# Optimization experiments

Measured on AMD Instinct MI355X. Metric: run time of the kernel, lower is better.

## Reference

```python
import jax, jax.numpy as jnp
import numpy as np

N, M = 8192, 128  # n samples, m features


def setup_inputs() -> dict:
    key = jax.random.key(0)
    k0, k1, k2, k3, k4 = jax.random.split(key, 5)
    L = jax.random.normal(k0, (N, M), dtype=jnp.float32)
    X = jax.random.normal(k1, (N, M), dtype=jnp.float32)
    Y = jax.random.normal(k2, (N,), dtype=jnp.float32)
    # params of the sub-network `net` (modeled as Linear(m, m))
    Wnet = jax.random.normal(k3, (M, M), dtype=jnp.float32) / np.float32(np.sqrt(M))
    bnet = jax.random.normal(k4, (M,), dtype=jnp.float32) * 0.01
    return {"L": L, "X": X, "Y": Y, "Wnet": Wnet, "bnet": bnet}


def reference(L, X, Y, Wnet, bnet):
    # A[i] = L[i] * X[i];  B[j] = net(X[j]) * X[j]   (elementwise feature weighting)
    A = L * X                                    # [n, m]
    B = (X @ Wnet + bnet) * X                    # [n, m] -- net(X[j]) computed once, batched
    # pairwise L2 distances: dist[i,j] = ||A_i - B_j||
    d2 = (jnp.sum(A * A, axis=1)[:, None]
          + jnp.sum(B * B, axis=1)[None, :]
          - 2.0 * (A @ B.T))                     # [n, n]
    dist = jnp.sqrt(jnp.maximum(d2, 1e-12))
    drum = jnp.exp(-dist)                        # [n, n] kernel weights
    # Nadaraya-Watson prediction: pred_i = (drum_i . Y) / sum_j drum_ij
    pred = (drum @ Y) / jnp.sum(drum, axis=1)    # [n]
    return jnp.sum((Y - pred) ** 2)              # scalar loss
```

## Files before the change

### kernel.cpp

```cpp
#include <hip/hip_runtime.h>
#include <hip/hip_bf16.h>
#include <cstdint>


#define N_ 8192
#define M_ 128
#define K2_ 2.0813689810056077f
#define NEG2K2_ -4.1627379620112154f

typedef __bf16 bf16x8 __attribute__((ext_vector_type(8)));
typedef float  f32x4  __attribute__((ext_vector_type(4)));

__device__ __forceinline__ unsigned short f2bf(float f) {
    unsigned int x = __float_as_uint(f);
    unsigned int r = x + 0x7fffu + ((x >> 16) & 1u);
    return (unsigned short)(r >> 16);
}

__device__ __forceinline__ void async_cp16(const void* g, void* l) {
    __builtin_amdgcn_global_load_lds(
        (const __attribute__((address_space(1))) void*)g,
        (__attribute__((address_space(3))) void*)l, 16, 0, 0);
}


__global__ __launch_bounds__(256) void prep_kernel(
    const float* __restrict__ L, const float* __restrict__ X,
    const float* __restrict__ Y, const float* __restrict__ Wnet,
    const float* __restrict__ bnet,
    unsigned short* __restrict__ Asw, unsigned short* __restrict__ Bsw,
    float* __restrict__ naS, float2* __restrict__ nbY,
    float* __restrict__ sumw, float* __restrict__ sumwy)
{
    __shared__ float Xs[16][128];
    const int tid  = threadIdx.x;
    const int row0 = blockIdx.x * 16;
    const int k4   = tid & 31;
    const int rr   = tid >> 5;

    #pragma unroll
    for (int i = 0; i < 2; ++i)
        ((float4*)Xs)[tid + i * 256] =
            ((const float4*)(X + (size_t)row0 * 128))[tid + i * 256];
    __syncthreads();

    float acc0[4] = {0.f, 0.f, 0.f, 0.f};
    float acc1[4] = {0.f, 0.f, 0.f, 0.f};
    const int r0 = rr * 2, r1 = rr * 2 + 1;
    #pragma unroll 4
    for (int c = 0; c < 128; ++c) {
        float4 w4 = *(const float4*)(Wnet + c * 128 + k4 * 4);
        float x0 = Xs[r0][c], x1 = Xs[r1][c];
        acc0[0] = fmaf(x0, w4.x, acc0[0]); acc1[0] = fmaf(x1, w4.x, acc1[0]);
        acc0[1] = fmaf(x0, w4.y, acc0[1]); acc1[1] = fmaf(x1, w4.y, acc1[1]);
        acc0[2] = fmaf(x0, w4.z, acc0[2]); acc1[2] = fmaf(x1, w4.z, acc1[2]);
        acc0[3] = fmaf(x0, w4.w, acc0[3]); acc1[3] = fmaf(x1, w4.w, acc1[3]);
    }

    const float4 bn4 = *(const float4*)(bnet + k4 * 4);
    float napart[2], nbpart[2];
    #pragma unroll
    for (int j = 0; j < 2; ++j) {
        const int ln  = rr * 2 + j;
        const int row = row0 + ln;
        const float* acc = j ? acc1 : acc0;
        const float4 xv = *(const float4*)(&Xs[ln][k4 * 4]);
        const float4 l4 = *(const float4*)(L + (size_t)row * 128 + k4 * 4);
        unsigned short apk[4], bpk[4];
        float nA_ = 0.f, nB_ = 0.f;
        const float xe[4] = {xv.x, xv.y, xv.z, xv.w};
        const float le[4] = {l4.x, l4.y, l4.z, l4.w};
        const float be[4] = {bn4.x, bn4.y, bn4.z, bn4.w};
        #pragma unroll
        for (int e = 0; e < 4; ++e) {
            float a = le[e] * xe[e];
            float b = (acc[e] + be[e]) * xe[e];
            unsigned short ua = f2bf(a), ub = f2bf(b);
            apk[e] = ua; bpk[e] = ub;
            float af = __uint_as_float((unsigned)ua << 16);
            float bf = __uint_as_float((unsigned)ub << 16);
            nA_ = fmaf(af, af, nA_);
            nB_ = fmaf(bf, bf, nB_);
        }
        napart[j] = nA_; nbpart[j] = nB_;
        size_t off = (size_t)blockIdx.x * 2048 + (size_t)(k4 >> 3) * 512
                   + (size_t)((k4 >> 1) & 3) * 128 + (size_t)ln * 8 + (k4 & 1) * 4;
        uint2 pa = make_uint2((unsigned)apk[0] | ((unsigned)apk[1] << 16),
                              (unsigned)apk[2] | ((unsigned)apk[3] << 16));
        uint2 pb = make_uint2((unsigned)bpk[0] | ((unsigned)bpk[1] << 16),
                              (unsigned)bpk[2] | ((unsigned)bpk[3] << 16));
        *(uint2*)(Asw + off) = pa;
        *(uint2*)(Bsw + off) = pb;
    }

    #pragma unroll
    for (int m = 1; m <= 16; m <<= 1) {
        napart[0] += __shfl_xor(napart[0], m, 64);
        napart[1] += __shfl_xor(napart[1], m, 64);
        nbpart[0] += __shfl_xor(nbpart[0], m, 64);
        nbpart[1] += __shfl_xor(nbpart[1], m, 64);
    }
    if (k4 == 0) {
        #pragma unroll
        for (int j = 0; j < 2; ++j) {
            int row = row0 + rr * 2 + j;
            naS[row] = K2_ * napart[j];
            nbY[row] = make_float2(K2_ * nbpart[j], Y[row]);
        }
    }
    if (tid < 16) sumw[row0 + tid] = 0.f;
    else if (tid < 32) sumwy[row0 + tid - 16] = 0.f;
}

__global__ __launch_bounds__(256) void pairwise_kernel(
    const unsigned short* __restrict__ Asw, const unsigned short* __restrict__ Bsw,
    const float* __restrict__ naS, const float2* __restrict__ nbY,
    float* __restrict__ sumw, float* __restrict__ sumwy)
{
    __shared__ __align__(16) unsigned short ldsB[16384];
    __shared__ __align__(16) float2 ldsNbY[512];

    const int tid  = threadIdx.x;
    const int wv   = tid >> 6;
    const int lane = tid & 63;
    const int ln16 = lane & 15;
    const int quad = lane >> 4;
    const int i0   = blockIdx.x * 128;
    const int j0   = blockIdx.y * 512;

    ((float4*)ldsNbY)[tid] = ((const float4*)(nbY + j0))[tid];

    bf16x8 afrag[2][4];
    float  na[2][4];
    #pragma unroll
    for (int rt = 0; rt < 2; ++rt) {
        const int gA = (i0 >> 4) + wv * 2 + rt;
        const unsigned short* ap = Asw + (size_t)gA * 2048 + lane * 8;
        #pragma unroll
        for (int ks = 0; ks < 4; ++ks)
            afrag[rt][ks] = *(const bf16x8*)(ap + ks * 512);
        #pragma unroll
        for (int r = 0; r < 4; ++r)
            na[rt][r] = naS[gA * 16 + quad * 4 + r];
    }

    float accw[2][4], accwy[2][4];
    #pragma unroll
    for (int rt = 0; rt < 2; ++rt)
        #pragma unroll
        for (int r = 0; r < 4; ++r) { accw[rt][r] = 0.f; accwy[rt][r] = 0.f; }

    for (int jt = 0; jt < 4; ++jt) {
        {
            const unsigned short* gsrc = Bsw + (size_t)(j0 >> 4) * 2048
                                       + (size_t)jt * 16384 + wv * 4096 + lane * 8;
            unsigned short* ldst = ldsB + wv * 4096;
            #pragma unroll
            for (int i = 0; i < 8; ++i)
                async_cp16(gsrc + i * 512, ldst + i * 512);
        }
        __syncthreads();

        #pragma unroll 2
        for (int ct = 0; ct < 8; ++ct) {
            bf16x8 bfrag[4];
            const unsigned short* bp = ldsB + ct * 2048 + lane * 8;
            #pragma unroll
            for (int ks = 0; ks < 4; ++ks)
                bfrag[ks] = *(const bf16x8*)(bp + ks * 512);
            const float2 nv = ldsNbY[jt * 128 + ct * 16 + ln16];

            #pragma unroll
            for (int rt = 0; rt < 2; ++rt) {
                f32x4 s = {0.f, 0.f, 0.f, 0.f};
                #pragma unroll
                for (int ks = 0; ks < 4; ++ks)
                    s = __builtin_amdgcn_mfma_f32_16x16x32_bf16(
                            afrag[rt][ks], bfrag[ks], s, 0, 0, 0);
                #pragma unroll
                for (int r = 0; r < 4; ++r) {
                    float d2 = fmaf(NEG2K2_, s[r], na[rt][r] + nv.x);
                    d2 = fmaxf(d2, 0.f);
                    float w = __builtin_amdgcn_exp2f(-__builtin_amdgcn_sqrtf(d2));
                    accw[rt][r] += w;
                    accwy[rt][r] = fmaf(w, nv.y, accwy[rt][r]);
                }
            }
        }
        __syncthreads();
    }

    #pragma unroll
    for (int rt = 0; rt < 2; ++rt)
        #pragma unroll
        for (int r = 0; r < 4; ++r) {
            float w  = accw[rt][r];
            float wy = accwy[rt][r];
            #pragma unroll
            for (int m = 1; m <= 8; m <<= 1) {
                w  += __shfl_xor(w,  m, 64);
                wy += __shfl_xor(wy, m, 64);
            }
            if (ln16 == 0) {
                int row = i0 + wv * 32 + rt * 16 + quad * 4 + r;
                atomicAdd(&sumw[row],  w);
                atomicAdd(&sumwy[row], wy);
            }
        }
}

__global__ __launch_bounds__(1024) void finish_kernel(
    const float* __restrict__ Y, const float* __restrict__ sumw,
    const float* __restrict__ sumwy, float* __restrict__ out)
{
    __shared__ float red[16];
    const int tid = threadIdx.x;
    float acc = 0.f;
    #pragma unroll
    for (int i = 0; i < 2; ++i) {
        int idx = tid + i * 1024;
        float4 w4  = ((const float4*)sumw)[idx];
        float4 wy4 = ((const float4*)sumwy)[idx];
        float4 y4  = ((const float4*)Y)[idx];
        const float we[4]  = {w4.x, w4.y, w4.z, w4.w};
        const float wye[4] = {wy4.x, wy4.y, wy4.z, wy4.w};
        const float ye[4]  = {y4.x, y4.y, y4.z, y4.w};
        #pragma unroll
        for (int e = 0; e < 4; ++e) {
            float pred = wye[e] * __builtin_amdgcn_rcpf(we[e]);
            float d = ye[e] - pred;
            acc = fmaf(d, d, acc);
        }
    }
    #pragma unroll
    for (int m = 1; m < 64; m <<= 1) acc += __shfl_xor(acc, m, 64);
    if ((tid & 63) == 0) red[tid >> 6] = acc;
    __syncthreads();
    if (tid < 64) {
        float v = (tid < 16) ? red[tid] : 0.f;
        #pragma unroll
        for (int m = 1; m < 16; m <<= 1) v += __shfl_xor(v, m, 64);
        if (tid == 0) out[0] = v;
    }
}

extern "C" void kernel_launch(void* const* d_in, const int* in_sizes, int n_in,
                              void* d_out, int out_size, void* d_ws, size_t ws_size,
                              hipStream_t stream)
{
    const float* L    = (const float*)d_in[0];
    const float* X    = (const float*)d_in[1];
    const float* Y    = (const float*)d_in[2];
    const float* Wnet = (const float*)d_in[3];
    const float* bnet = (const float*)d_in[4];
    float* out = (float*)d_out;

    char* ws = (char*)d_ws;
    unsigned short* Asw = (unsigned short*)(ws);
    unsigned short* Bsw = (unsigned short*)(ws + (size_t)2 * 1024 * 1024);
    float*  naS   = (float*) (ws + (size_t)4 * 1024 * 1024);
    float2* nbYp  = (float2*)(ws + (size_t)4 * 1024 * 1024 + 32 * 1024);
    float*  sumw  = (float*) (ws + (size_t)4 * 1024 * 1024 + 96 * 1024);
    float*  sumwy = (float*) (ws + (size_t)4 * 1024 * 1024 + 128 * 1024);

    prep_kernel<<<N_ / 16, 256, 0, stream>>>(L, X, Y, Wnet, bnet,
                                             Asw, Bsw, naS, nbYp, sumw, sumwy);
    pairwise_kernel<<<dim3(N_ / 128, 16), 256, 0, stream>>>(Asw, Bsw, naS, nbYp,
                                                            sumw, sumwy);
    finish_kernel<<<1, 1024, 0, stream>>>(Y, sumw, sumwy, out);
}
```

Measured before the change: 105.6 us.

## Load B fragments directly from global memory and stage Wnet in LDS

The pairwise kernel drops its LDS staging of B tiles and nbY, along with the barriers, and instead loads MFMA B fragments and norms directly from global memory (cached) inside one 32-iteration loop. It also sets a launch-bounds occupancy hint of 4 blocks per CU. The prep kernel copies the whole Wnet matrix into 64KB of LDS and reads four columns at a time with vector loads. The goals are to remove barrier stalls and async-copy overhead and to raise occupancy, at the cost of relying on L1/L2 to hold the B fragments that every wave re-reads.

```diff
diff --git a/kernel.cpp b/kernel.cpp
--- a/kernel.cpp
+++ b/kernel.cpp
@@ -15,12 +15,6 @@
     unsigned int x = __float_as_uint(f);
     unsigned int r = x + 0x7fffu + ((x >> 16) & 1u);
     return (unsigned short)(r >> 16);
-}
-
-__device__ __forceinline__ void async_cp16(const void* g, void* l) {
-    __builtin_amdgcn_global_load_lds(
-        (const __attribute__((address_space(1))) void*)g,
-        (__attribute__((address_space(3))) void*)l, 16, 0, 0);
 }
 
 
@@ -32,6 +26,7 @@
     float* __restrict__ naS, float2* __restrict__ nbY,
     float* __restrict__ sumw, float* __restrict__ sumwy)
 {
+    __shared__ float Ws[128 * 128];
     __shared__ float Xs[16][128];
     const int tid  = threadIdx.x;
     const int row0 = blockIdx.x * 16;
@@ -39,6 +34,9 @@
     const int rr   = tid >> 5;
 
     #pragma unroll
+    for (int i = 0; i < 16; ++i)
+        ((float4*)Ws)[tid + i * 256] = ((const float4*)Wnet)[tid + i * 256];
+    #pragma unroll
     for (int i = 0; i < 2; ++i)
         ((float4*)Xs)[tid + i * 256] =
             ((const float4*)(X + (size_t)row0 * 128))[tid + i * 256];
@@ -47,14 +45,28 @@
     float acc0[4] = {0.f, 0.f, 0.f, 0.f};
     float acc1[4] = {0.f, 0.f, 0.f, 0.f};
     const int r0 = rr * 2, r1 = rr * 2 + 1;
-    #pragma unroll 4
-    for (int c = 0; c < 128; ++c) {
-        float4 w4 = *(const float4*)(Wnet + c * 128 + k4 * 4);
-        float x0 = Xs[r0][c], x1 = Xs[r1][c];
-        acc0[0] = fmaf(x0, w4.x, acc0[0]); acc1[0] = fmaf(x1, w4.x, acc1[0]);
-        acc0[1] = fmaf(x0, w4.y, acc0[1]); acc1[1] = fmaf(x1, w4.y, acc1[1]);
-        acc0[2] = fmaf(x0, w4.z, acc0[2]); acc1[2] = fmaf(x1, w4.z, acc1[2]);
-        acc0[3] = fmaf(x0, w4.w, acc0[3]); acc1[3] = fmaf(x1, w4.w, acc1[3]);
+    #pragma unroll 2
+    for (int c4 = 0; c4 < 128; c4 += 4) {
+        const float4 x0 = *(const float4*)&Xs[r0][c4];
+        const float4 x1 = *(const float4*)&Xs[r1][c4];
+        const float4 wc0 = *(const float4*)&Ws[(c4 + 0) * 128 + k4 * 4];
+        const float4 wc1 = *(const float4*)&Ws[(c4 + 1) * 128 + k4 * 4];
+        const float4 wc2 = *(const float4*)&Ws[(c4 + 2) * 128 + k4 * 4];
+        const float4 wc3 = *(const float4*)&Ws[(c4 + 3) * 128 + k4 * 4];
+        const float x0e[4] = {x0.x, x0.y, x0.z, x0.w};
+        const float x1e[4] = {x1.x, x1.y, x1.z, x1.w};
+        const float4 wce[4] = {wc0, wc1, wc2, wc3};
+        #pragma unroll
+        for (int c = 0; c < 4; ++c) {
+            acc0[0] = fmaf(x0e[c], wce[c].x, acc0[0]);
+            acc0[1] = fmaf(x0e[c], wce[c].y, acc0[1]);
+            acc0[2] = fmaf(x0e[c], wce[c].z, acc0[2]);
+            acc0[3] = fmaf(x0e[c], wce[c].w, acc0[3]);
+            acc1[0] = fmaf(x1e[c], wce[c].x, acc1[0]);
+            acc1[1] = fmaf(x1e[c], wce[c].y, acc1[1]);
+            acc1[2] = fmaf(x1e[c], wce[c].z, acc1[2]);
+            acc1[3] = fmaf(x1e[c], wce[c].w, acc1[3]);
+        }
     }
 
     const float4 bn4 = *(const float4*)(bnet + k4 * 4);
@@ -112,14 +124,11 @@
     else if (tid < 32) sumwy[row0 + tid - 16] = 0.f;
 }
 
-__global__ __launch_bounds__(256) void pairwise_kernel(
+__global__ __launch_bounds__(256, 4) void pairwise_kernel(
     const unsigned short* __restrict__ Asw, const unsigned short* __restrict__ Bsw,
     const float* __restrict__ naS, const float2* __restrict__ nbY,
     float* __restrict__ sumw, float* __restrict__ sumwy)
 {
-    __shared__ __align__(16) unsigned short ldsB[16384];
-    __shared__ __align__(16) float2 ldsNbY[512];
-
     const int tid  = threadIdx.x;
     const int wv   = tid >> 6;
     const int lane = tid & 63;
@@ -128,8 +137,6 @@
     const int i0   = blockIdx.x * 128;
     const int j0   = blockIdx.y * 512;
 
-    ((float4*)ldsNbY)[tid] = ((const float4*)(nbY + j0))[tid];
-
     bf16x8 afrag[2][4];
     float  na[2][4];
     #pragma unroll
@@ -150,44 +157,34 @@
         #pragma unroll
         for (int r = 0; r < 4; ++r) { accw[rt][r] = 0.f; accwy[rt][r] = 0.f; }
 
-    for (int jt = 0; jt < 4; ++jt) {
-        {
-            const unsigned short* gsrc = Bsw + (size_t)(j0 >> 4) * 2048
-                                       + (size_t)jt * 16384 + wv * 4096 + lane * 8;
-            unsigned short* ldst = ldsB + wv * 4096;
-            #pragma unroll
-            for (int i = 0; i < 8; ++i)
-                async_cp16(gsrc + i * 512, ldst + i * 512);
-        }
-        __syncthreads();
-
-        #pragma unroll 2
-        for (int ct = 0; ct < 8; ++ct) {
-            bf16x8 bfrag[4];
-            const unsigned short* bp = ldsB + ct * 2048 + lane * 8;
+    const unsigned short* bbase = Bsw + (size_t)(j0 >> 4) * 2048 + lane * 8;
+    const float2* nbbase = nbY + j0 + ln16;
+
+    #pragma unroll 4
+    for (int ct = 0; ct < 32; ++ct) {
+        const unsigned short* bp = bbase + (size_t)ct * 2048;
+        bf16x8 bfrag[4];
+        #pragma unroll
+        for (int ks = 0; ks < 4; ++ks)
+            bfrag[ks] = *(const bf16x8*)(bp + ks * 512);
+        const float2 nv = nbbase[ct * 16];
+
+        #pragma unroll
+        for (int rt = 0; rt < 2; ++rt) {
+            f32x4 s = {0.f, 0.f, 0.f, 0.f};
             #pragma unroll
             for (int ks = 0; ks < 4; ++ks)
-                bfrag[ks] = *(const bf16x8*)(bp + ks * 512);
-            const float2 nv = ldsNbY[jt * 128 + ct * 16 + ln16];
-
+                s = __builtin_amdgcn_mfma_f32_16x16x32_bf16(
+                        afrag[rt][ks], bfrag[ks], s, 0, 0, 0);
             #pragma unroll
-            for (int rt = 0; rt < 2; ++rt) {
-                f32x4 s = {0.f, 0.f, 0.f, 0.f};
-                #pragma unroll
-                for (int ks = 0; ks < 4; ++ks)
-                    s = __builtin_amdgcn_mfma_f32_16x16x32_bf16(
-                            afrag[rt][ks], bfrag[ks], s, 0, 0, 0);
-                #pragma unroll
-                for (int r = 0; r < 4; ++r) {
-                    float d2 = fmaf(NEG2K2_, s[r], na[rt][r] + nv.x);
-                    d2 = fmaxf(d2, 0.f);
-                    float w = __builtin_amdgcn_exp2f(-__builtin_amdgcn_sqrtf(d2));
-                    accw[rt][r] += w;
-                    accwy[rt][r] = fmaf(w, nv.y, accwy[rt][r]);
-                }
+            for (int r = 0; r < 4; ++r) {
+                float d2 = fmaf(NEG2K2_, s[r], na[rt][r] + nv.x);
+                d2 = fmaxf(d2, 0.f);
+                float w = __builtin_amdgcn_exp2f(-__builtin_amdgcn_sqrtf(d2));
+                accw[rt][r] += w;
+                accwy[rt][r] = fmaf(w, nv.y, accwy[rt][r]);
             }
         }
-        __syncthreads();
     }
 
     #pragma unroll
```

After: 105.5 us. Within noise of the previous version (-0.1%).

## Drop LDS staging in pairwise kernel, load B fragments directly with register double-buffering

Applied to the files above, without the earlier changes.

The pairwise kernel no longer stages B tiles into LDS with async copies and barriers. Each wave now reads its B fragments straight from global memory (L2) into two register buffers that are prefetched one step ahead. Each block covers 64 rows instead of 128 with one row tile per wave, and the kernel gets an occupancy hint of 6. The prep kernel moves to 64-thread blocks with a 4x8 register tile and packs bf16 pairs with 16-byte stores. The trade is more L2 traffic per block and a doubled grid, in return for no barriers and higher occupancy.

```diff
diff --git a/kernel.cpp b/kernel.cpp
--- a/kernel.cpp
+++ b/kernel.cpp
@@ -4,27 +4,23 @@
 
 
 #define N_ 8192
-#define M_ 128
 #define K2_ 2.0813689810056077f
 #define NEG2K2_ -4.1627379620112154f
 
 typedef __bf16 bf16x8 __attribute__((ext_vector_type(8)));
 typedef float  f32x4  __attribute__((ext_vector_type(4)));
 
-__device__ __forceinline__ unsigned short f2bf(float f) {
-    unsigned int x = __float_as_uint(f);
-    unsigned int r = x + 0x7fffu + ((x >> 16) & 1u);
-    return (unsigned short)(r >> 16);
-}
-
-__device__ __forceinline__ void async_cp16(const void* g, void* l) {
-    __builtin_amdgcn_global_load_lds(
-        (const __attribute__((address_space(1))) void*)g,
-        (__attribute__((address_space(3))) void*)l, 16, 0, 0);
-}
-
-
-__global__ __launch_bounds__(256) void prep_kernel(
+
+__device__ __forceinline__ uint32_t rne2(float f0, float f1, float& r0, float& r1) {
+    uint32_t u0 = __float_as_uint(f0), u1 = __float_as_uint(f1);
+    uint32_t t0 = u0 + 0x7fffu + ((u0 >> 16) & 1u);
+    uint32_t t1 = u1 + 0x7fffu + ((u1 >> 16) & 1u);
+    r0 = __uint_as_float(t0 & 0xffff0000u);
+    r1 = __uint_as_float(t1 & 0xffff0000u);
+    return (t0 >> 16) | (t1 & 0xffff0000u);
+}
+
+__global__ __launch_bounds__(64) void prep_kernel(
     const float* __restrict__ L, const float* __restrict__ X,
     const float* __restrict__ Y, const float* __restrict__ Wnet,
     const float* __restrict__ bnet,
@@ -35,178 +31,192 @@
     __shared__ float Xs[16][128];
     const int tid  = threadIdx.x;
     const int row0 = blockIdx.x * 16;
-    const int k4   = tid & 31;
-    const int rr   = tid >> 5;
-
-    #pragma unroll
-    for (int i = 0; i < 2; ++i)
-        ((float4*)Xs)[tid + i * 256] =
-            ((const float4*)(X + (size_t)row0 * 128))[tid + i * 256];
+    const int rg   = tid >> 4;
+    const int cg   = tid & 15;
+
+    #pragma unroll
+    for (int i = 0; i < 8; ++i)
+        ((float4*)Xs)[tid + i * 64] =
+            ((const float4*)(X + (size_t)row0 * 128))[tid + i * 64];
+    if (tid < 16) sumw[row0 + tid] = 0.f;
+    else if (tid < 32) sumwy[row0 + tid - 16] = 0.f;
     __syncthreads();
 
-    float acc0[4] = {0.f, 0.f, 0.f, 0.f};
-    float acc1[4] = {0.f, 0.f, 0.f, 0.f};
-    const int r0 = rr * 2, r1 = rr * 2 + 1;
+    float acc[4][8];
+    #pragma unroll
+    for (int r = 0; r < 4; ++r)
+        #pragma unroll
+        for (int e = 0; e < 8; ++e) acc[r][e] = 0.f;
+
     #pragma unroll 4
     for (int c = 0; c < 128; ++c) {
-        float4 w4 = *(const float4*)(Wnet + c * 128 + k4 * 4);
-        float x0 = Xs[r0][c], x1 = Xs[r1][c];
-        acc0[0] = fmaf(x0, w4.x, acc0[0]); acc1[0] = fmaf(x1, w4.x, acc1[0]);
-        acc0[1] = fmaf(x0, w4.y, acc0[1]); acc1[1] = fmaf(x1, w4.y, acc1[1]);
-        acc0[2] = fmaf(x0, w4.z, acc0[2]); acc1[2] = fmaf(x1, w4.z, acc1[2]);
-        acc0[3] = fmaf(x0, w4.w, acc0[3]); acc1[3] = fmaf(x1, w4.w, acc1[3]);
-    }
-
-    const float4 bn4 = *(const float4*)(bnet + k4 * 4);
-    float napart[2], nbpart[2];
-    #pragma unroll
-    for (int j = 0; j < 2; ++j) {
-        const int ln  = rr * 2 + j;
+        const float4 w0 = *(const float4*)(Wnet + c * 128 + cg * 8);
+        const float4 w1 = *(const float4*)(Wnet + c * 128 + cg * 8 + 4);
+        const float we[8] = {w0.x, w0.y, w0.z, w0.w, w1.x, w1.y, w1.z, w1.w};
+        #pragma unroll
+        for (int r = 0; r < 4; ++r) {
+            const float xv = Xs[rg * 4 + r][c];
+            #pragma unroll
+            for (int e = 0; e < 8; ++e)
+                acc[r][e] = fmaf(xv, we[e], acc[r][e]);
+        }
+    }
+
+    const float4 bn0 = *(const float4*)(bnet + cg * 8);
+    const float4 bn1 = *(const float4*)(bnet + cg * 8 + 4);
+    const float bne[8] = {bn0.x, bn0.y, bn0.z, bn0.w, bn1.x, bn1.y, bn1.z, bn1.w};
+    const int ks = cg >> 2, quad = cg & 3;
+
+    float napart[4], nbpart[4];
+    #pragma unroll
+    for (int r = 0; r < 4; ++r) {
+        const int ln  = rg * 4 + r;
         const int row = row0 + ln;
-        const float* acc = j ? acc1 : acc0;
-        const float4 xv = *(const float4*)(&Xs[ln][k4 * 4]);
-        const float4 l4 = *(const float4*)(L + (size_t)row * 128 + k4 * 4);
-        unsigned short apk[4], bpk[4];
-        float nA_ = 0.f, nB_ = 0.f;
-        const float xe[4] = {xv.x, xv.y, xv.z, xv.w};
-        const float le[4] = {l4.x, l4.y, l4.z, l4.w};
-        const float be[4] = {bn4.x, bn4.y, bn4.z, bn4.w};
-        #pragma unroll
-        for (int e = 0; e < 4; ++e) {
-            float a = le[e] * xe[e];
-            float b = (acc[e] + be[e]) * xe[e];
-            unsigned short ua = f2bf(a), ub = f2bf(b);
-            apk[e] = ua; bpk[e] = ub;
-            float af = __uint_as_float((unsigned)ua << 16);
-            float bf = __uint_as_float((unsigned)ub << 16);
-            nA_ = fmaf(af, af, nA_);
-            nB_ = fmaf(bf, bf, nB_);
-        }
-        napart[j] = nA_; nbpart[j] = nB_;
-        size_t off = (size_t)blockIdx.x * 2048 + (size_t)(k4 >> 3) * 512
-                   + (size_t)((k4 >> 1) & 3) * 128 + (size_t)ln * 8 + (k4 & 1) * 4;
-        uint2 pa = make_uint2((unsigned)apk[0] | ((unsigned)apk[1] << 16),
-                              (unsigned)apk[2] | ((unsigned)apk[3] << 16));
-        uint2 pb = make_uint2((unsigned)bpk[0] | ((unsigned)bpk[1] << 16),
-                              (unsigned)bpk[2] | ((unsigned)bpk[3] << 16));
-        *(uint2*)(Asw + off) = pa;
-        *(uint2*)(Bsw + off) = pb;
-    }
-
-    #pragma unroll
-    for (int m = 1; m <= 16; m <<= 1) {
-        napart[0] += __shfl_xor(napart[0], m, 64);
-        napart[1] += __shfl_xor(napart[1], m, 64);
-        nbpart[0] += __shfl_xor(nbpart[0], m, 64);
-        nbpart[1] += __shfl_xor(nbpart[1], m, 64);
-    }
-    if (k4 == 0) {
-        #pragma unroll
-        for (int j = 0; j < 2; ++j) {
-            int row = row0 + rr * 2 + j;
-            naS[row] = K2_ * napart[j];
-            nbY[row] = make_float2(K2_ * nbpart[j], Y[row]);
-        }
-    }
-    if (tid < 16) sumw[row0 + tid] = 0.f;
-    else if (tid < 32) sumwy[row0 + tid - 16] = 0.f;
-}
-
-__global__ __launch_bounds__(256) void pairwise_kernel(
+        const float4 x0 = *(const float4*)(&Xs[ln][cg * 8]);
+        const float4 x1 = *(const float4*)(&Xs[ln][cg * 8 + 4]);
+        const float4 l0 = *(const float4*)(L + (size_t)row * 128 + cg * 8);
+        const float4 l1 = *(const float4*)(L + (size_t)row * 128 + cg * 8 + 4);
+        const float xe[8] = {x0.x, x0.y, x0.z, x0.w, x1.x, x1.y, x1.z, x1.w};
+        const float le[8] = {l0.x, l0.y, l0.z, l0.w, l1.x, l1.y, l1.z, l1.w};
+        uint32_t pa[4], pb[4];
+        float na_ = 0.f, nb_ = 0.f;
+        #pragma unroll
+        for (int h = 0; h < 4; ++h) {
+            float a0 = le[2 * h] * xe[2 * h];
+            float a1 = le[2 * h + 1] * xe[2 * h + 1];
+            float b0 = (acc[r][2 * h] + bne[2 * h]) * xe[2 * h];
+            float b1 = (acc[r][2 * h + 1] + bne[2 * h + 1]) * xe[2 * h + 1];
+            float ra0, ra1, rb0, rb1;
+            pa[h] = rne2(a0, a1, ra0, ra1);
+            pb[h] = rne2(b0, b1, rb0, rb1);
+            na_ = fmaf(ra0, ra0, na_); na_ = fmaf(ra1, ra1, na_);
+            nb_ = fmaf(rb0, rb0, nb_); nb_ = fmaf(rb1, rb1, nb_);
+        }
+        napart[r] = na_; nbpart[r] = nb_;
+        size_t off = (size_t)blockIdx.x * 2048 + (size_t)ks * 512
+                   + (size_t)quad * 128 + (size_t)ln * 8;
+        *(uint4*)(Asw + off) = make_uint4(pa[0], pa[1], pa[2], pa[3]);
+        *(uint4*)(Bsw + off) = make_uint4(pb[0], pb[1], pb[2], pb[3]);
+    }
+
+    #pragma unroll
+    for (int m = 1; m <= 8; m <<= 1) {
+        #pragma unroll
+        for (int r = 0; r < 4; ++r) {
+            napart[r] += __shfl_xor(napart[r], m, 64);
+            nbpart[r] += __shfl_xor(nbpart[r], m, 64);
+        }
+    }
+    if (cg == 0) {
+        #pragma unroll
+        for (int r = 0; r < 4; ++r) {
+            int row = row0 + rg * 4 + r;
+            naS[row] = K2_ * napart[r];
+            nbY[row] = make_float2(K2_ * nbpart[r], Y[row]);
+        }
+    }
+}
+
+__global__ __launch_bounds__(256, 6) void pairwise_kernel(
     const unsigned short* __restrict__ Asw, const unsigned short* __restrict__ Bsw,
     const float* __restrict__ naS, const float2* __restrict__ nbY,
     float* __restrict__ sumw, float* __restrict__ sumwy)
 {
-    __shared__ __align__(16) unsigned short ldsB[16384];
-    __shared__ __align__(16) float2 ldsNbY[512];
-
     const int tid  = threadIdx.x;
     const int wv   = tid >> 6;
     const int lane = tid & 63;
     const int ln16 = lane & 15;
     const int quad = lane >> 4;
-    const int i0   = blockIdx.x * 128;
+    const int i0   = blockIdx.x * 64;
     const int j0   = blockIdx.y * 512;
-
-    ((float4*)ldsNbY)[tid] = ((const float4*)(nbY + j0))[tid];
-
-    bf16x8 afrag[2][4];
-    float  na[2][4];
-    #pragma unroll
-    for (int rt = 0; rt < 2; ++rt) {
-        const int gA = (i0 >> 4) + wv * 2 + rt;
+    const int gA   = (i0 >> 4) + wv;
+
+    bf16x8 afrag[4];
+    {
         const unsigned short* ap = Asw + (size_t)gA * 2048 + lane * 8;
         #pragma unroll
-        for (int ks = 0; ks < 4; ++ks)
-            afrag[rt][ks] = *(const bf16x8*)(ap + ks * 512);
-        #pragma unroll
-        for (int r = 0; r < 4; ++r)
-            na[rt][r] = naS[gA * 16 + quad * 4 + r];
-    }
-
-    float accw[2][4], accwy[2][4];
-    #pragma unroll
-    for (int rt = 0; rt < 2; ++rt)
-        #pragma unroll
-        for (int r = 0; r < 4; ++r) { accw[rt][r] = 0.f; accwy[rt][r] = 0.f; }
-
-    for (int jt = 0; jt < 4; ++jt) {
+        for (int ksi = 0; ksi < 4; ++ksi)
+            afrag[ksi] = *(const bf16x8*)(ap + ksi * 512);
+    }
+    float na[4];
+    #pragma unroll
+    for (int r = 0; r < 4; ++r)
+        na[r] = naS[gA * 16 + quad * 4 + r];
+
+    float accw[4] = {0.f, 0.f, 0.f, 0.f};
+    float accwy[4] = {0.f, 0.f, 0.f, 0.f};
+
+    const unsigned short* bbase = Bsw + (size_t)(j0 >> 4) * 2048 + lane * 8;
+    const float2* nbb = nbY + j0 + ln16;
+
+    bf16x8 b0[4], b1[4];
+    float2 nv0, nv1;
+    #pragma unroll
+    for (int ksi = 0; ksi < 4; ++ksi) {
+        b0[ksi] = *(const bf16x8*)(bbase + ksi * 512);
+        b1[ksi] = *(const bf16x8*)(bbase + 2048 + ksi * 512);
+    }
+    nv0 = nbb[0];
+    nv1 = nbb[16];
+
+    for (int ct = 0; ct < 32; ct += 2) {
         {
-            const unsigned short* gsrc = Bsw + (size_t)(j0 >> 4) * 2048
-                                       + (size_t)jt * 16384 + wv * 4096 + lane * 8;
-            unsigned short* ldst = ldsB + wv * 4096;
-            #pragma unroll
-            for (int i = 0; i < 8; ++i)
-                async_cp16(gsrc + i * 512, ldst + i * 512);
-        }
-        __syncthreads();
-
-        #pragma unroll 2
-        for (int ct = 0; ct < 8; ++ct) {
-            bf16x8 bfrag[4];
-            const unsigned short* bp = ldsB + ct * 2048 + lane * 8;
-            #pragma unroll
-            for (int ks = 0; ks < 4; ++ks)
-                bfrag[ks] = *(const bf16x8*)(bp + ks * 512);
-            const float2 nv = ldsNbY[jt * 128 + ct * 16 + ln16];
-
-            #pragma unroll
-            for (int rt = 0; rt < 2; ++rt) {
-                f32x4 s = {0.f, 0.f, 0.f, 0.f};
-                #pragma unroll
-                for (int ks = 0; ks < 4; ++ks)
-                    s = __builtin_amdgcn_mfma_f32_16x16x32_bf16(
-                            afrag[rt][ks], bfrag[ks], s, 0, 0, 0);
-                #pragma unroll
-                for (int r = 0; r < 4; ++r) {
-                    float d2 = fmaf(NEG2K2_, s[r], na[rt][r] + nv.x);
-                    d2 = fmaxf(d2, 0.f);
-                    float w = __builtin_amdgcn_exp2f(-__builtin_amdgcn_sqrtf(d2));
-                    accw[rt][r] += w;
-                    accwy[rt][r] = fmaf(w, nv.y, accwy[rt][r]);
-                }
+            f32x4 s = {0.f, 0.f, 0.f, 0.f};
+            #pragma unroll
+            for (int ksi = 0; ksi < 4; ++ksi)
+                s = __builtin_amdgcn_mfma_f32_16x16x32_bf16(afrag[ksi], b0[ksi], s, 0, 0, 0);
+            const unsigned short* bp = bbase + (size_t)(ct + 2) * 2048;
+            const float yj = nv0.y, nb = nv0.x;
+            #pragma unroll
+            for (int ksi = 0; ksi < 4; ++ksi)
+                b0[ksi] = *(const bf16x8*)(bp + ksi * 512);
+            nv0 = nbb[(ct + 2) * 16];
+            #pragma unroll
+            for (int r = 0; r < 4; ++r) {
+                float d2 = fmaf(NEG2K2_, s[r], na[r] + nb);
+                d2 = fmaxf(d2, 0.f);
+                float w = __builtin_amdgcn_exp2f(-__builtin_amdgcn_sqrtf(d2));
+                accw[r] += w;
+                accwy[r] = fmaf(w, yj, accwy[r]);
             }
         }
-        __syncthreads();
-    }
-
-    #pragma unroll
-    for (int rt = 0; rt < 2; ++rt)
-        #pragma unroll
-        for (int r = 0; r < 4; ++r) {
-            float w  = accw[rt][r];
-            float wy = accwy[rt][r];
-            #pragma unroll
-            for (int m = 1; m <= 8; m <<= 1) {
-                w  += __shfl_xor(w,  m, 64);
-                wy += __shfl_xor(wy, m, 64);
+        {
+            f32x4 s = {0.f, 0.f, 0.f, 0.f};
+            #pragma unroll
+            for (int ksi = 0; ksi < 4; ++ksi)
+                s = __builtin_amdgcn_mfma_f32_16x16x32_bf16(afrag[ksi], b1[ksi], s, 0, 0, 0);
+            const unsigned short* bp = bbase + (size_t)(ct + 3) * 2048;
+            const float yj = nv1.y, nb = nv1.x;
+            #pragma unroll
+            for (int ksi = 0; ksi < 4; ++ksi)
+                b1[ksi] = *(const bf16x8*)(bp + ksi * 512);
+            nv1 = nbb[(ct + 3) * 16];
+            #pragma unroll
+            for (int r = 0; r < 4; ++r) {
+                float d2 = fmaf(NEG2K2_, s[r], na[r] + nb);
+                d2 = fmaxf(d2, 0.f);
+                float w = __builtin_amdgcn_exp2f(-__builtin_amdgcn_sqrtf(d2));
+                accw[r] += w;
+                accwy[r] = fmaf(w, yj, accwy[r]);
             }
-            if (ln16 == 0) {
-                int row = i0 + wv * 32 + rt * 16 + quad * 4 + r;
-                atomicAdd(&sumw[row],  w);
-                atomicAdd(&sumwy[row], wy);
-            }
-        }
+        }
+    }
+
+    #pragma unroll
+    for (int r = 0; r < 4; ++r) {
+        float w  = accw[r];
+        float wy = accwy[r];
+        #pragma unroll
+        for (int m = 1; m <= 8; m <<= 1) {
+            w  += __shfl_xor(w,  m, 64);
+            wy += __shfl_xor(wy, m, 64);
+        }
+        if (ln16 == 0) {
+            int row = i0 + wv * 16 + quad * 4 + r;
+            atomicAdd(&sumw[row],  w);
+            atomicAdd(&sumwy[row], wy);
+        }
+    }
 }
 
 __global__ __launch_bounds__(1024) void finish_kernel(
@@ -263,9 +273,9 @@
     float*  sumw  = (float*) (ws + (size_t)4 * 1024 * 1024 + 96 * 1024);
     float*  sumwy = (float*) (ws + (size_t)4 * 1024 * 1024 + 128 * 1024);
 
-    prep_kernel<<<N_ / 16, 256, 0, stream>>>(L, X, Y, Wnet, bnet,
-                                             Asw, Bsw, naS, nbYp, sumw, sumwy);
-    pairwise_kernel<<<dim3(N_ / 128, 16), 256, 0, stream>>>(Asw, Bsw, naS, nbYp,
-                                                            sumw, sumwy);
+    prep_kernel<<<N_ / 16, 64, 0, stream>>>(L, X, Y, Wnet, bnet,
+                                            Asw, Bsw, naS, nbYp, sumw, sumwy);
+    pairwise_kernel<<<dim3(N_ / 64, 16), 256, 0, stream>>>(Asw, Bsw, naS, nbYp,
+                                                           sumw, sumwy);
     finish_kernel<<<1, 1024, 0, stream>>>(Y, sumw, sumwy, out);
 }
```

After: 130.5 us. 1.24x slower.
